# Kernel tuning notes

Measured on AMD Instinct MI355X. Metric: run time of the kernel, lower is better.

The kernel has to match this reference:

```python
import jax, jax.numpy as jnp
import numpy as np

# ---- dims (match init_kwargs) ----
N_E, N_R = 200000, 500
DIM_C, DIM_L, DIM_D = 64, 256, 128
NUM_LAYERS, N_HEADS = 2, 4
FEAT = 2 * DIM_D + DIM_C          # event embedding dim = 320
IN_DIM = FEAT + DIM_D + 1         # attention input: evt + time_emb + ones = 449
DH = FEAT // N_HEADS              # head dim = 80
B, T = 32, 64
TIME_M, TIME_MAX = 1.0, 2000.0
EPS = 1e-8


def setup_inputs() -> dict:
    key = jax.random.key(0)
    ks = jax.random.split(key, 18)
    s = 0.05
    seq_subject = jax.random.randint(ks[0], (B, T), 0, N_E)
    seq_object = jax.random.randint(ks[1], (B, T), 0, N_E)
    seq_relation = jax.random.randint(ks[2], (B, T), 0, N_R)
    # chronological event times
    seq_time = jnp.cumsum(jax.random.uniform(ks[3], (B, T)) * 2.0, axis=1)
    # persistent entity memory buffers
    mem = jax.random.normal(ks[4], (N_E, DIM_D)) * 0.1
    latest_time = jnp.zeros((N_E,), jnp.float32)
    # relation embedding table with padding row (idx N_R) zeroed
    relation_emb = (jax.random.normal(ks[5], (N_R + 1, DIM_C)) * 0.1).at[N_R].set(0.0)
    # RNN entity update params (torch Linear, bias=False; stored as [in,out])
    W_hidden = jax.random.normal(ks[6], (2 * DIM_D + DIM_C, DIM_L)) * s
    W_hh = jax.random.normal(ks[7], (DIM_L, DIM_D)) * s
    W_st = jax.random.normal(ks[8], (DIM_D,)) * s
    W_ot = jax.random.normal(ks[9], (DIM_D,)) * s
    # stacked ANHP multi-head attention params per layer
    att_Wq = jax.random.normal(ks[10], (NUM_LAYERS, IN_DIM, N_HEADS * DH)) * s
    att_Wk = jax.random.normal(ks[11], (NUM_LAYERS, IN_DIM, N_HEADS * DH)) * s
    att_Wv = jax.random.normal(ks[12], (NUM_LAYERS, IN_DIM, N_HEADS * DH)) * s
    att_Wo = jax.random.normal(ks[13], (NUM_LAYERS, N_HEADS * DH, FEAT)) * s
    # score MLP: Linear(FEAT, DIM_D) -> ReLU -> Linear(DIM_D, 1)
    score_W1 = jax.random.normal(ks[14], (FEAT, DIM_D)) * s
    score_b1 = jnp.zeros((DIM_D,), jnp.float32)
    score_W2 = jax.random.normal(ks[15], (DIM_D, 1)) * s
    score_b2 = jnp.zeros((1,), jnp.float32)
    return dict(seq_subject=seq_subject, seq_object=seq_object,
                seq_relation=seq_relation, seq_time=seq_time,
                mem=mem, latest_time=latest_time, relation_emb=relation_emb,
                W_hidden=W_hidden, W_hh=W_hh, W_st=W_st, W_ot=W_ot,
                att_Wq=att_Wq, att_Wk=att_Wk, att_Wv=att_Wv, att_Wo=att_Wo,
                score_W1=score_W1, score_b1=score_b1,
                score_W2=score_W2, score_b2=score_b2)


def _forward(seq_subject, seq_object, seq_relation, seq_time,
             mem, latest_time, relation_emb,
             W_hidden, W_hh, W_st, W_ot,
             att_Wq, att_Wk, att_Wv, att_Wo,
             score_W1, score_b1, score_W2, score_b2):
    # ---- phase 1: sequential gather -> RNN update -> scatter over entity memory ----
    def step(carry, x):
        m, lt = carry
        s, o, r, t = x                      # each [B]
        s_emb = m[s]                        # gather [B, DIM_D]
        o_emb = m[o]
        r_emb = relation_emb[r]             # [B, DIM_C]
        inp = jnp.concatenate([s_emb, o_emb, r_emb], -1)   # [B, 2d+c]
        h = jax.nn.sigmoid(inp @ W_hidden)                  # [B, DIM_L]
        dt_s = t - lt[s]
        dt_o = t - lt[o]
        hh = h @ W_hh                                       # [B, DIM_D]
        new_s = jax.nn.sigmoid(dt_s[:, None] * W_st[None, :] + hh)
        new_o = jax.nn.sigmoid(dt_o[:, None] * W_ot[None, :] + hh)
        m = m.at[s].set(new_s).at[o].set(new_o)             # scatter back
        lt = lt.at[s].set(t).at[o].set(t)
        evt = jnp.concatenate([new_s, new_o, r_emb], -1)    # [B, FEAT]
        return (m, lt), evt

    xs = (seq_subject.T, seq_object.T, seq_relation.T, seq_time.T)  # [T, B]
    (mem, latest_time), evt_seq = jax.lax.scan(step, (mem, latest_time), xs)
    evt = jnp.transpose(evt_seq, (1, 0, 2))                 # [B, T, FEAT]

    # ---- phase 2: temporal attention scoring (causal: event i attends to j < i) ----
    norm = 1.0 / (TIME_M * (5.0 * TIME_MAX / TIME_M) ** jnp.arange(DIM_D, dtype=jnp.float32))
    time_emb = jnp.sin(seq_time[..., None] * norm)          # [B, T, DIM_D]
    ones = jnp.ones(evt.shape[:-1] + (1,), evt.dtype)
    causal = jnp.tril(jnp.ones((T, T), bool), -1)           # strict past mask
    scale = 1.0 / np.sqrt(DH)

    x = evt
    for l in range(NUM_LAYERS):
        e = jnp.concatenate([x, time_emb, ones], -1)        # [B, T, IN_DIM]
        q = (e @ att_Wq[l]).reshape(B, T, N_HEADS, DH)
        k = (e @ att_Wk[l]).reshape(B, T, N_HEADS, DH)
        v = (e @ att_Wv[l]).reshape(B, T, N_HEADS, DH)
        scores = jnp.einsum('bqhd,bkhd->bhqk', q, k) * scale
        scores = jnp.where(causal, scores, -1e9)
        attn = jax.nn.softmax(scores, axis=-1) * causal     # row 0 (no past) -> zero update
        out = jnp.einsum('bhqk,bkhd->bqhd', attn, v).reshape(B, T, N_HEADS * DH)
        x = x + jnp.tanh(out @ att_Wo[l])

    score = (jax.nn.relu(x @ score_W1 + score_b1) @ score_W2 + score_b2)[..., 0]  # [B, T]
    lam = jax.nn.softplus(score)                             # event intensities
    loss = -jnp.log(lam + EPS)
    total_loss = jnp.mean(loss)                              # mean over batch, averaged /T per step
    return total_loss, lam, mem, latest_time


def reference(seq_subject, seq_object, seq_relation, seq_time,
              mem, latest_time, relation_emb,
              W_hidden, W_hh, W_st, W_ot,
              att_Wq, att_Wk, att_Wv, att_Wo,
              score_W1, score_b1, score_W2, score_b2):
    return _forward(seq_subject, seq_object, seq_relation, seq_time,
                    mem, latest_time, relation_emb,
                    W_hidden, W_hh, W_st, W_ot,
                    att_Wq, att_Wk, att_Wv, att_Wo,
                    score_W1, score_b1, score_W2, score_b2)
```

## Files before the change

### kernel.cpp

```cpp
#include <hip/hip_runtime.h>

#define NE   200000
#define DC   64
#define DL   256
#define DD   128
#define FEAT 320
#define IND  449
#define INDP 512
#define DH   80
#define BB   32
#define TT   64
#define NEV  2048
#define NSLOT 4096

typedef __attribute__((ext_vector_type(4))) float  floatx4;
typedef __attribute__((ext_vector_type(4), aligned(4))) float floatx4u;

__device__ __forceinline__ float sigmoidf_(float x) { return 1.0f / (1.0f + __expf(-x)); }

__global__ __launch_bounds__(256)
void copy_init(const float* __restrict__ mem0, const float* __restrict__ lt0,
               float* __restrict__ out_mem, float* __restrict__ out_lt) {
    const size_t NM = (size_t)NE * DD;
    const size_t NL = (size_t)NE;
    size_t gid = (size_t)blockIdx.x * 256 + threadIdx.x;
    size_t stride = (size_t)gridDim.x * 256;
    if (gid == 0) {
        out_mem[0] = mem0[0]; out_mem[1] = mem0[1]; out_mem[2] = mem0[2];
        out_mem[NM - 1] = mem0[NM - 1];
        out_lt[0] = lt0[0]; out_lt[1] = lt0[1]; out_lt[2] = lt0[2];
        out_lt[NL - 1] = lt0[NL - 1];
    }
    const size_t nm4 = (NM - 4) / 4;
    float* __restrict__ dm = out_mem + 3;
    size_t i = gid;
    for (; i + 3 * stride < nm4; i += 4 * stride) {
        size_t i0 = i, i1 = i + stride, i2 = i + 2 * stride, i3 = i + 3 * stride;
        floatx4 lo0 = __builtin_nontemporal_load((const floatx4*)&mem0[i0 * 4]);
        floatx4 hi0 = __builtin_nontemporal_load((const floatx4*)&mem0[i0 * 4 + 4]);
        floatx4 lo1 = __builtin_nontemporal_load((const floatx4*)&mem0[i1 * 4]);
        floatx4 hi1 = __builtin_nontemporal_load((const floatx4*)&mem0[i1 * 4 + 4]);
        floatx4 lo2 = __builtin_nontemporal_load((const floatx4*)&mem0[i2 * 4]);
        floatx4 hi2 = __builtin_nontemporal_load((const floatx4*)&mem0[i2 * 4 + 4]);
        floatx4 lo3 = __builtin_nontemporal_load((const floatx4*)&mem0[i3 * 4]);
        floatx4 hi3 = __builtin_nontemporal_load((const floatx4*)&mem0[i3 * 4 + 4]);
        floatx4 o0 = {lo0[3], hi0[0], hi0[1], hi0[2]};
        floatx4 o1 = {lo1[3], hi1[0], hi1[1], hi1[2]};
        floatx4 o2 = {lo2[3], hi2[0], hi2[1], hi2[2]};
        floatx4 o3 = {lo3[3], hi3[0], hi3[1], hi3[2]};
        __builtin_nontemporal_store(o0, (floatx4*)&dm[i0 * 4]);
        __builtin_nontemporal_store(o1, (floatx4*)&dm[i1 * 4]);
        __builtin_nontemporal_store(o2, (floatx4*)&dm[i2 * 4]);
        __builtin_nontemporal_store(o3, (floatx4*)&dm[i3 * 4]);
    }
    for (; i < nm4; i += stride) {
        floatx4 lo = __builtin_nontemporal_load((const floatx4*)&mem0[i * 4]);
        floatx4 hi = __builtin_nontemporal_load((const floatx4*)&mem0[i * 4 + 4]);
        floatx4 o = {lo[3], hi[0], hi[1], hi[2]};
        __builtin_nontemporal_store(o, (floatx4*)&dm[i * 4]);
    }
    const size_t nl4 = (NL - 4) / 4;
    float* __restrict__ dl = out_lt + 3;
    for (size_t j = gid; j < nl4; j += stride) {
        floatx4 lo = __builtin_nontemporal_load((const floatx4*)&lt0[j * 4]);
        floatx4 hi = __builtin_nontemporal_load((const floatx4*)&lt0[j * 4 + 4]);
        floatx4 o = {lo[3], hi[0], hi[1], hi[2]};
        __builtin_nontemporal_store(o, (floatx4*)&dl[j * 4]);
    }
}

__global__ __launch_bounds__(256)
void slot_analyze(const int* __restrict__ seq_s, const int* __restrict__ seq_o,
                  const float* __restrict__ seq_time, const float* __restrict__ lt0,
                  float* __restrict__ slotDt, int* __restrict__ slotPrev,
                  int* __restrict__ slotWin) {
    __shared__ int entL[NSLOT];
    int tid = threadIdx.x;
    for (int j = tid; j < NSLOT; j += 256) {
        int b = j & 31, side = (j >> 5) & 1, t = j >> 6;
        entL[j] = (side ? seq_o : seq_s)[b * TT + t];
    }
    __syncthreads();
    int wave = tid >> 6, lane = tid & 63;
    int slot = blockIdx.x * 4 + wave;
    int t = slot >> 6;
    int myent = entL[slot];
    int win = 1, best = -1;
#pragma unroll 8
    for (int jj = 0; jj < NSLOT / 64; ++jj) {
        int j = jj * 64 + lane;
        if (entL[j] == myent) {
            if (j > slot) win = 0;
            else if ((j >> 6) < t && j > best) best = j;
        }
    }
#pragma unroll
    for (int off = 32; off; off >>= 1) {
        int ob = __shfl_xor(best, off, 64);
        best = best > ob ? best : ob;
    }
    win = __all(win);
    if (lane == 0) {
        int b = slot & 31;
        float tv = seq_time[b * TT + t];
        float pt = (best >= 0) ? seq_time[(best & 31) * TT + (best >> 6)] : lt0[myent];
        slotDt[slot]   = tv - pt;
        slotPrev[slot] = best;
        slotWin[slot]  = win;
    }
}

__global__ __launch_bounds__(256)
void fixlist_build(const int* __restrict__ slotPrev, int* __restrict__ fixList,
                   int* __restrict__ fixState, int* __restrict__ evFixIdx,
                   int* __restrict__ fixCnt) {
    int e = blockIdx.x * 256 + threadIdx.x;
    int b = e >> 6, t = e & 63;
    int c = (slotPrev[t * 64 + b] >= 0) | (slotPrev[t * 64 + 32 + b] >= 0);
    int idx = -1;
    if (c) { idx = atomicAdd(fixCnt, 1); fixList[idx] = e; fixState[idx] = -1; }
    evFixIdx[e] = idx;
}

__global__ __launch_bounds__(256)
void event_compute(const int* __restrict__ seq_s, const int* __restrict__ seq_o,
                   const int* __restrict__ seq_r, const float* __restrict__ seq_time,
                   const float* __restrict__ mem0, const float* __restrict__ rel,
                   const float* __restrict__ W_hidden, const float* __restrict__ W_hh,
                   const float* __restrict__ W_st, const float* __restrict__ W_ot,
                   const float* __restrict__ slotDt,
                   float* __restrict__ evt, float* __restrict__ ebuf) {
    __shared__ float xc[8][FEAT];
    __shared__ float hs[8][DL];
    __shared__ int   sSi[8], sOi[8], sRi[8];
    __shared__ float sDs[8], sDo[8], sTv[8];
    int tid = threadIdx.x;
    int e0 = blockIdx.x * 8;
    if (tid < 8) {
        int e = e0 + tid;
        sSi[tid] = seq_s[e]; sOi[tid] = seq_o[e]; sRi[tid] = seq_r[e];
        int b = e >> 6, t = e & 63;
        sDs[tid] = slotDt[t * 64 + b];
        sDo[tid] = slotDt[t * 64 + 32 + b];
        sTv[tid] = seq_time[e];
    }
    __syncthreads();
    for (int i = tid; i < 8 * FEAT; i += 256) {
        int r = i / FEAT, k = i - r * FEAT;
        float v;
        if (k < DD)            v = mem0[(size_t)sSi[r] * DD + k];
        else if (k < 2 * DD)   v = mem0[(size_t)sOi[r] * DD + (k - DD)];
        else                   v = rel[(size_t)sRi[r] * DC + (k - 2 * DD)];
        xc[r][k] = v;
    }
    __syncthreads();
    {
        int j = tid;
        float acc[8] = {0.f,0.f,0.f,0.f,0.f,0.f,0.f,0.f};
        for (int k = 0; k < FEAT; ++k) {
            float w = W_hidden[(size_t)k * DL + j];
#pragma unroll
            for (int r = 0; r < 8; ++r) acc[r] += xc[r][k] * w;
        }
#pragma unroll
        for (int r = 0; r < 8; ++r) hs[r][j] = sigmoidf_(acc[r]);
    }
    __syncthreads();
    {
        int d = tid & 127, grp = tid >> 7;
        float acc[4] = {0.f,0.f,0.f,0.f};
        for (int l = 0; l < DL; ++l) {
            float w = W_hh[(size_t)l * DD + d];
#pragma unroll
            for (int rr = 0; rr < 4; ++rr) acc[rr] += hs[grp * 4 + rr][l] * w;
        }
        float wst = W_st[d], wot = W_ot[d];
#pragma unroll
        for (int rr = 0; rr < 4; ++rr) {
            int r = grp * 4 + rr;
            int e = e0 + r;
            float ns  = sigmoidf_(sDs[r] * wst + acc[rr]);
            float no_ = sigmoidf_(sDo[r] * wot + acc[rr]);
            evt[(size_t)e * FEAT + d]      = ns;
            evt[(size_t)e * FEAT + DD + d] = no_;
            ebuf[(size_t)e * INDP + d]      = ns;
            ebuf[(size_t)e * INDP + DD + d] = no_;
        }
    }
    for (int i = tid; i < 8 * DC; i += 256) {
        int r = i >> 6, c = i & 63;
        float v = xc[r][2 * DD + c];
        int e = e0 + r;
        evt[(size_t)e * FEAT + 2 * DD + c] = v;
        ebuf[(size_t)e * INDP + 2 * DD + c] = v;
    }
    for (int i = tid; i < 8 * DD; i += 256) {
        int r = i >> 7, d = i & 127;
        float denom = __powf(1.0e4f, (float)d);
        float v = sinf(sTv[r] * (1.0f / denom));
        int e = e0 + r;
        ebuf[(size_t)e * INDP + FEAT + d] = v;
    }
    if (tid < 8) ebuf[(size_t)(e0 + tid) * INDP + FEAT + DD] = 1.0f;
}

__global__ __launch_bounds__(256)
void fix_round(int round,
               const int* __restrict__ seq_s, const int* __restrict__ seq_o,
               const float* __restrict__ mem0, const float* __restrict__ W_hidden,
               const float* __restrict__ W_hh, const float* __restrict__ W_st,
               const float* __restrict__ W_ot, const float* __restrict__ slotDt,
               const int* __restrict__ slotPrev, const int* __restrict__ fixList,
               int* __restrict__ fixState, const int* __restrict__ evFixIdx,
               const int* __restrict__ fixCnt,
               float* __restrict__ evt, float* __restrict__ ebuf) {
    __shared__ float xc[FEAT];
    __shared__ float hsv[DL];
    __shared__ float hp[2][DD];
    __shared__ int sGo, sPs, sPo, sE;
    int tid = threadIdx.x;
    int n = *fixCnt;
    for (int f = blockIdx.x; f < n; f += gridDim.x) {
        if (tid == 0) {
            int go = 0, ps = 0, po = 0, e = 0;
            if (fixState[f] == -1) {
                e = fixList[f];
                int b = e >> 6, t = e & 63;
                ps = slotPrev[t * 64 + b];
                po = slotPrev[t * 64 + 32 + b];
                go = 1;
                if (ps >= 0) {
                    int pe = (ps & 31) * 64 + (ps >> 6);
                    int fi = evFixIdx[pe];
                    if (fi >= 0) { int st = fixState[fi]; if (st < 0 || st >= round) go = 0; }
                }
                if (po >= 0) {
                    int pe = (po & 31) * 64 + (po >> 6);
                    int fi = evFixIdx[pe];
                    if (fi >= 0) { int st = fixState[fi]; if (st < 0 || st >= round) go = 0; }
                }
            }
            sGo = go; sPs = ps; sPo = po; sE = e;
        }
        __syncthreads();
        int go = sGo, ps = sPs, po = sPo, e = sE;
        __syncthreads();
        if (!go) continue;
        int b = e >> 6, t = e & 63;
        for (int i = tid; i < FEAT; i += 256) {
            float v;
            if (i < DD) {
                v = (ps >= 0) ? evt[(size_t)((ps & 31) * 64 + (ps >> 6)) * FEAT + ((ps >> 5) & 1) * DD + i]
                              : mem0[(size_t)seq_s[e] * DD + i];
            } else if (i < 2 * DD) {
                int k = i - DD;
                v = (po >= 0) ? evt[(size_t)((po & 31) * 64 + (po >> 6)) * FEAT + ((po >> 5) & 1) * DD + k]
                              : mem0[(size_t)seq_o[e] * DD + k];
            } else {
                v = evt[(size_t)e * FEAT + i];
            }
            xc[i] = v;
        }
        __syncthreads();
        {
            float a0 = 0.f, a1 = 0.f, a2 = 0.f, a3 = 0.f;
            for (int k = 0; k < FEAT; k += 4) {
                a0 += xc[k]     * W_hidden[(size_t)k * DL + tid];
                a1 += xc[k + 1] * W_hidden[(size_t)(k + 1) * DL + tid];
                a2 += xc[k + 2] * W_hidden[(size_t)(k + 2) * DL + tid];
                a3 += xc[k + 3] * W_hidden[(size_t)(k + 3) * DL + tid];
            }
            hsv[tid] = sigmoidf_((a0 + a1) + (a2 + a3));
        }
        __syncthreads();
        {
            int d = tid & 127, g = tid >> 7;
            float a0 = 0.f, a1 = 0.f;
            int l0 = g * 128;
            for (int l = 0; l < 128; l += 2) {
                a0 += hsv[l0 + l]     * W_hh[(size_t)(l0 + l) * DD + d];
                a1 += hsv[l0 + l + 1] * W_hh[(size_t)(l0 + l + 1) * DD + d];
            }
            hp[g][d] = a0 + a1;
        }
        __syncthreads();
        if (tid < DD) {
            float hh = hp[0][tid] + hp[1][tid];
            float ns  = sigmoidf_(slotDt[t * 64 + b]      * W_st[tid] + hh);
            float no_ = sigmoidf_(slotDt[t * 64 + 32 + b] * W_ot[tid] + hh);
            evt[(size_t)e * FEAT + tid]      = ns;
            evt[(size_t)e * FEAT + DD + tid] = no_;
            ebuf[(size_t)e * INDP + tid]      = ns;
            ebuf[(size_t)e * INDP + DD + tid] = no_;
        }
        __syncthreads();
        __threadfence();
        if (tid == 0) fixState[f] = round;
        __syncthreads();
    }
}

__global__ __launch_bounds__(256)
void scatter_win(const int* __restrict__ seq_s, const int* __restrict__ seq_o,
                 const float* __restrict__ seq_time, const int* __restrict__ slotWin,
                 const float* __restrict__ evt, float* __restrict__ out_mem,
                 float* __restrict__ out_lt) {
    int gid = blockIdx.x * 256 + threadIdx.x;
    int slot = gid >> 5, c = gid & 31;
    if (!slotWin[slot]) return;
    int b = slot & 31, side = (slot >> 5) & 1, t = slot >> 6;
    int e = b * TT + t;
    int ent = (side ? seq_o : seq_s)[e];
    floatx4 v = *(const floatx4*)&evt[(size_t)e * FEAT + side * DD + c * 4];
    *(floatx4u*)&out_mem[(size_t)ent * DD + c * 4] = v;
    if (c == 0) out_lt[ent] = seq_time[e];
}

__global__ __launch_bounds__(128)
void proj(const float* __restrict__ ebuf, const float* __restrict__ Wq,
          const float* __restrict__ Wk, const float* __restrict__ Wv,
          float* __restrict__ q, float* __restrict__ k, float* __restrict__ v) {
    __shared__ float AsT[2][32][33];
    __shared__ float Bs[2][32][36];
    __shared__ float comb[32][36];
    const float* W = (blockIdx.z == 0) ? Wq : (blockIdx.z == 1) ? Wk : Wv;
    float* out = (blockIdx.z == 0) ? q : (blockIdx.z == 1) ? k : v;
    int tid = threadIdx.x;
    int w = tid >> 6, lane = tid & 63;
    int row0 = blockIdx.x * 32, col0 = blockIdx.y * 32;
    int tx = lane & 7, ty = lane >> 3;
    const int sr = lane >> 3, sk4 = (lane & 7) * 4;
    const int IT0 = w * 8, IT1 = IT0 + 8;
    floatx4 aR[4], bR[4], acc[4];
#pragma unroll
    for (int i = 0; i < 4; ++i) acc[i] = (floatx4){0.f, 0.f, 0.f, 0.f};
#pragma unroll
    for (int m = 0; m < 4; ++m) {
        int r = m * 8 + sr;
        int kg = IT0 * 32 + r;
        aR[m] = *(const floatx4*)&ebuf[(size_t)(row0 + r) * INDP + IT0 * 32 + sk4];
        bR[m] = (kg < IND) ? *(const floatx4*)&W[(size_t)kg * FEAT + col0 + sk4]
                           : (floatx4){0.f, 0.f, 0.f, 0.f};
    }
    for (int it = IT0; it < IT1; ++it) {
        __syncthreads();
#pragma unroll
        for (int m = 0; m < 4; ++m) {
            int r = m * 8 + sr;
            AsT[w][sk4 + 0][r] = aR[m][0];
            AsT[w][sk4 + 1][r] = aR[m][1];
            AsT[w][sk4 + 2][r] = aR[m][2];
            AsT[w][sk4 + 3][r] = aR[m][3];
            *(floatx4*)&Bs[w][r][sk4] = bR[m];
        }
        __syncthreads();
        if (it + 1 < IT1) {
            int k0n = (it + 1) * 32;
#pragma unroll
            for (int m = 0; m < 4; ++m) {
                int r = m * 8 + sr;
                int kg = k0n + r;
                aR[m] = *(const floatx4*)&ebuf[(size_t)(row0 + r) * INDP + k0n + sk4];
                bR[m] = (kg < IND) ? *(const floatx4*)&W[(size_t)kg * FEAT + col0 + sk4]
                                   : (floatx4){0.f, 0.f, 0.f, 0.f};
            }
        }
#pragma unroll
        for (int kk = 0; kk < 32; ++kk) {
            floatx4 a = *(const floatx4*)&AsT[w][kk][ty * 4];
            floatx4 b = *(const floatx4*)&Bs[w][kk][tx * 4];
#pragma unroll
            for (int i = 0; i < 4; ++i) acc[i] += a[i] * b;
        }
    }
    if (w == 1) {
#pragma unroll
        for (int i = 0; i < 4; ++i)
            *(floatx4*)&comb[ty * 4 + i][tx * 4] = acc[i];
    }
    __syncthreads();
    if (w == 0) {
#pragma unroll
        for (int i = 0; i < 4; ++i) {
            floatx4 p = *(const floatx4*)&comb[ty * 4 + i][tx * 4];
            floatx4 s = acc[i] + p;
            *(floatx4*)&out[(size_t)(row0 + ty * 4 + i) * FEAT + col0 + tx * 4] = s;
        }
    }
}

__global__ __launch_bounds__(128)
void outproj(const float* __restrict__ ain, const float* __restrict__ Wo,
             const float* __restrict__ resid, float* __restrict__ xout,
             float* __restrict__ ebufW, int writeE) {
    __shared__ float AsT[2][32][33];
    __shared__ float Bs[2][32][36];
    __shared__ float comb[32][36];
    int tid = threadIdx.x;
    int w = tid >> 6, lane = tid & 63;
    int row0 = blockIdx.x * 32, col0 = blockIdx.y * 32;
    int tx = lane & 7, ty = lane >> 3;
    const int sr = lane >> 3, sk4 = (lane & 7) * 4;
    const int IT0 = w * 5, IT1 = IT0 + 5;
    floatx4 aR[4], bR[4], acc[4];
#pragma unroll
    for (int i = 0; i < 4; ++i) acc[i] = (floatx4){0.f, 0.f, 0.f, 0.f};
#pragma unroll
    for (int m = 0; m < 4; ++m) {
        int r = m * 8 + sr;
        aR[m] = *(const floatx4*)&ain[(size_t)(row0 + r) * FEAT + IT0 * 32 + sk4];
        bR[m] = *(const floatx4*)&Wo[(size_t)(IT0 * 32 + r) * FEAT + col0 + sk4];
    }
    for (int it = IT0; it < IT1; ++it) {
        __syncthreads();
#pragma unroll
        for (int m = 0; m < 4; ++m) {
            int r = m * 8 + sr;
            AsT[w][sk4 + 0][r] = aR[m][0];
            AsT[w][sk4 + 1][r] = aR[m][1];
            AsT[w][sk4 + 2][r] = aR[m][2];
            AsT[w][sk4 + 3][r] = aR[m][3];
            *(floatx4*)&Bs[w][r][sk4] = bR[m];
        }
        __syncthreads();
        if (it + 1 < IT1) {
            int k0n = (it + 1) * 32;
#pragma unroll
            for (int m = 0; m < 4; ++m) {
                int r = m * 8 + sr;
                aR[m] = *(const floatx4*)&ain[(size_t)(row0 + r) * FEAT + k0n + sk4];
                bR[m] = *(const floatx4*)&Wo[(size_t)(k0n + r) * FEAT + col0 + sk4];
            }
        }
#pragma unroll
        for (int kk = 0; kk < 32; ++kk) {
            floatx4 a = *(const floatx4*)&AsT[w][kk][ty * 4];
            floatx4 b = *(const floatx4*)&Bs[w][kk][tx * 4];
#pragma unroll
            for (int i = 0; i < 4; ++i) acc[i] += a[i] * b;
        }
    }
    if (w == 1) {
#pragma unroll
        for (int i = 0; i < 4; ++i)
            *(floatx4*)&comb[ty * 4 + i][tx * 4] = acc[i];
    }
    __syncthreads();
    if (w == 0) {
#pragma unroll
        for (int i = 0; i < 4; ++i) {
            int row = row0 + ty * 4 + i;
            int c0 = col0 + tx * 4;
            floatx4 p = *(const floatx4*)&comb[ty * 4 + i][tx * 4];
            floatx4 a = acc[i] + p;
            floatx4 res = *(const floatx4*)&resid[(size_t)row * FEAT + c0];
            floatx4 o;
#pragma unroll
            for (int j = 0; j < 4; ++j) o[j] = res[j] + tanhf(a[j]);
            *(floatx4*)&xout[(size_t)row * FEAT + c0] = o;
            if (writeE) *(floatx4*)&ebufW[(size_t)row * INDP + c0] = o;
        }
    }
}

__global__ __launch_bounds__(256)
void attn(const float* __restrict__ q, const float* __restrict__ k,
          const float* __restrict__ v, float* __restrict__ ao) {
    __shared__ float qs[TT][DH], ks[TT][DH], vs[TT][DH];
    __shared__ float sc[TT][TT + 1];
    int bh = blockIdx.x;
    int b = bh >> 2, h = bh & 3;
    int tid = threadIdx.x;
    for (int i = tid; i < TT * DH; i += 256) {
        int r = i / DH, d = i - r * DH;
        size_t base = (size_t)(b * TT + r) * FEAT + h * DH + d;
        qs[r][d] = q[base]; ks[r][d] = k[base]; vs[r][d] = v[base];
    }
    __syncthreads();
    const float scale = 0.11180339887498949f;
    for (int idx = tid; idx < TT * TT; idx += 256) {
        int i = idx >> 6, j = idx & 63;
        float s = 0.f;
        for (int d = 0; d < DH; ++d) s += qs[i][d] * ks[j][d];
        sc[i][j] = s * scale;
    }
    __syncthreads();
    if (tid < TT) {
        int i = tid;
        if (i == 0) {
            for (int j = 0; j < TT; ++j) sc[0][j] = 0.0f;
        } else {
            float m = -1e30f;
            for (int j = 0; j < i; ++j) m = fmaxf(m, sc[i][j]);
            float sum = 0.f;
            for (int j = 0; j < i; ++j) { float p = __expf(sc[i][j] - m); sc[i][j] = p; sum += p; }
            float inv = 1.0f / sum;
            for (int j = 0; j < i; ++j) sc[i][j] *= inv;
            for (int j = i; j < TT; ++j) sc[i][j] = 0.0f;
        }
    }
    __syncthreads();
    for (int idx = tid; idx < TT * DH; idx += 256) {
        int i = idx / DH, d = idx - i * DH;
        float s = 0.f;
        for (int j = 0; j < TT; ++j) s += sc[i][j] * vs[j][d];
        ao[(size_t)(b * TT + i) * FEAT + h * DH + d] = s;
    }
}

__global__ __launch_bounds__(128)
void score_k(const float* __restrict__ x, const float* __restrict__ W1,
             const float* __restrict__ b1, const float* __restrict__ W2,
             const float* __restrict__ b2, float* __restrict__ lam_out,
             float* __restrict__ loss_out) {
    __shared__ float xr[FEAT];
    __shared__ float red[2];
    int e = blockIdx.x;
    int tid = threadIdx.x;
    for (int f = tid; f < FEAT; f += 128) xr[f] = x[(size_t)e * FEAT + f];
    __syncthreads();
    int d = tid;
    float acc = b1[d];
    for (int kk = 0; kk < FEAT; ++kk) acc += xr[kk] * W1[kk * DD + d];
    acc = fmaxf(acc, 0.0f) * W2[d];
    for (int off = 32; off; off >>= 1) acc += __shfl_down(acc, off, 64);
    if ((tid & 63) == 0) red[tid >> 6] = acc;
    __syncthreads();
    if (tid == 0) {
        float s = red[0] + red[1] + b2[0];
        float lam = fmaxf(s, 0.0f) + log1pf(expf(-fabsf(s)));
        lam_out[e] = lam;
        atomicAdd(loss_out, -logf(lam + 1e-8f) * (1.0f / 2048.0f));
    }
}

extern "C" void kernel_launch(void* const* d_in, const int* in_sizes, int n_in,
                              void* d_out, int out_size, void* d_ws, size_t ws_size,
                              hipStream_t stream) {
    const int*   seq_s = (const int*)d_in[0];
    const int*   seq_o = (const int*)d_in[1];
    const int*   seq_r = (const int*)d_in[2];
    const float* seq_t = (const float*)d_in[3];
    const float* mem0  = (const float*)d_in[4];
    const float* lt0   = (const float*)d_in[5];
    const float* rel   = (const float*)d_in[6];
    const float* W_hidden = (const float*)d_in[7];
    const float* W_hh  = (const float*)d_in[8];
    const float* W_st  = (const float*)d_in[9];
    const float* W_ot  = (const float*)d_in[10];
    const float* Wq    = (const float*)d_in[11];
    const float* Wk    = (const float*)d_in[12];
    const float* Wv    = (const float*)d_in[13];
    const float* Wo    = (const float*)d_in[14];
    const float* sW1   = (const float*)d_in[15];
    const float* sb1   = (const float*)d_in[16];
    const float* sW2   = (const float*)d_in[17];
    const float* sb2   = (const float*)d_in[18];

    float* out      = (float*)d_out;
    float* out_lam  = out + 1;
    float* out_mem  = out + 2049;
    float* out_lt   = out + 2049 + (size_t)NE * DD;

    float* ws = (float*)d_ws;
    float* evt   = ws;
    float* xbuf  = ws + 655360;
    float* ebuf  = ws + 1310720;
    float* qbuf  = ws + 2359296;
    float* kbuf  = ws + 3014656;
    float* vbuf  = ws + 3670016;
    float* aobuf = ws + 4325376;
    float* slotDt   = ws + 4980736;
    int*   slotPrev = (int*)(ws + 4984832);
    int*   slotWin  = (int*)(ws + 4988928);
    int*   fixList  = (int*)(ws + 4993024);
    int*   fixState = (int*)(ws + 4995072);
    int*   evFixIdx = (int*)(ws + 4997120);
    int*   fixCnt   = (int*)(ws + 4999168);

    hipMemsetAsync(fixCnt, 0, sizeof(int), stream);
    hipMemsetAsync(out, 0, sizeof(float), stream);
    hipMemsetAsync(ebuf, 0, (size_t)NEV * INDP * sizeof(float), stream);

    copy_init<<<2048, 256, 0, stream>>>(mem0, lt0, out_mem, out_lt);

    slot_analyze<<<NSLOT / 4, 256, 0, stream>>>(seq_s, seq_o, seq_t, lt0,
                                                slotDt, slotPrev, slotWin);
    fixlist_build<<<NEV / 256, 256, 0, stream>>>(slotPrev, fixList, fixState,
                                                 evFixIdx, fixCnt);
    event_compute<<<NEV / 8, 256, 0, stream>>>(seq_s, seq_o, seq_r, seq_t, mem0, rel,
                                               W_hidden, W_hh, W_st, W_ot, slotDt,
                                               evt, ebuf);
    for (int r = 0; r < 4; ++r)
        fix_round<<<64, 256, 0, stream>>>(r, seq_s, seq_o, mem0, W_hidden, W_hh,
                                          W_st, W_ot, slotDt, slotPrev,
                                          fixList, fixState, evFixIdx, fixCnt, evt, ebuf);
    scatter_win<<<512, 256, 0, stream>>>(seq_s, seq_o, seq_t, slotWin, evt, out_mem, out_lt);

    for (int l = 0; l < 2; ++l) {
        const float* src = l ? xbuf : evt;
        proj<<<dim3(64, 10, 3), 128, 0, stream>>>(ebuf,
                                                  Wq + (size_t)l * IND * FEAT,
                                                  Wk + (size_t)l * IND * FEAT,
                                                  Wv + (size_t)l * IND * FEAT,
                                                  qbuf, kbuf, vbuf);
        attn<<<128, 256, 0, stream>>>(qbuf, kbuf, vbuf, aobuf);
        outproj<<<dim3(64, 10), 128, 0, stream>>>(aobuf, Wo + (size_t)l * FEAT * FEAT,
                                                  src, xbuf, ebuf, (l == 0) ? 1 : 0);
    }
    score_k<<<NEV, 128, 0, stream>>>(xbuf, sW1, sb1, sW2, sb2, out_lam, out);
}
```

Before: 561.4 us.

## Split attention into query tiles, parallelize softmax with shuffles, pad shared arrays

```diff
diff --git a/kernel.cpp b/kernel.cpp
--- a/kernel.cpp
+++ b/kernel.cpp
@@ -466,45 +466,65 @@
 __global__ __launch_bounds__(256)
 void attn(const float* __restrict__ q, const float* __restrict__ k,
           const float* __restrict__ v, float* __restrict__ ao) {
-    __shared__ float qs[TT][DH], ks[TT][DH], vs[TT][DH];
-    __shared__ float sc[TT][TT + 1];
+    __shared__ float qs[16][80];
+    __shared__ float ks[TT][81];
+    __shared__ float vs[TT][81];
+    __shared__ float sc[16][65];
     int bh = blockIdx.x;
-    int b = bh >> 2, h = bh & 3;
+    int b = bh >> 4, h = (bh >> 2) & 3, qt = bh & 3;
     int tid = threadIdx.x;
     for (int i = tid; i < TT * DH; i += 256) {
         int r = i / DH, d = i - r * DH;
         size_t base = (size_t)(b * TT + r) * FEAT + h * DH + d;
-        qs[r][d] = q[base]; ks[r][d] = k[base]; vs[r][d] = v[base];
+        ks[r][d] = k[base];
+        vs[r][d] = v[base];
+    }
+    for (int i = tid; i < 16 * DH; i += 256) {
+        int r = i / DH, d = i - r * DH;
+        qs[r][d] = q[(size_t)(b * TT + qt * 16 + r) * FEAT + h * DH + d];
     }
     __syncthreads();
     const float scale = 0.11180339887498949f;
-    for (int idx = tid; idx < TT * TT; idx += 256) {
+    for (int idx = tid; idx < 16 * 64; idx += 256) {
         int i = idx >> 6, j = idx & 63;
         float s = 0.f;
+#pragma unroll 8
         for (int d = 0; d < DH; ++d) s += qs[i][d] * ks[j][d];
         sc[i][j] = s * scale;
     }
     __syncthreads();
-    if (tid < TT) {
-        int i = tid;
-        if (i == 0) {
-            for (int j = 0; j < TT; ++j) sc[0][j] = 0.0f;
-        } else {
-            float m = -1e30f;
-            for (int j = 0; j < i; ++j) m = fmaxf(m, sc[i][j]);
-            float sum = 0.f;
-            for (int j = 0; j < i; ++j) { float p = __expf(sc[i][j] - m); sc[i][j] = p; sum += p; }
-            float inv = 1.0f / sum;
-            for (int j = 0; j < i; ++j) sc[i][j] *= inv;
-            for (int j = i; j < TT; ++j) sc[i][j] = 0.0f;
-        }
-    }
-    __syncthreads();
-    for (int idx = tid; idx < TT * DH; idx += 256) {
+    {
+        int r = tid >> 4, l = tid & 15;
+        int qi = qt * 16 + r;
+        float p0, p1, p2, p3;
+        int j0 = l, j1 = l + 16, j2 = l + 32, j3 = l + 48;
+        p0 = (j0 < qi) ? sc[r][j0] : -1e30f;
+        p1 = (j1 < qi) ? sc[r][j1] : -1e30f;
+        p2 = (j2 < qi) ? sc[r][j2] : -1e30f;
+        p3 = (j3 < qi) ? sc[r][j3] : -1e30f;
+        float m = fmaxf(fmaxf(p0, p1), fmaxf(p2, p3));
+#pragma unroll
+        for (int off = 8; off; off >>= 1) m = fmaxf(m, __shfl_xor(m, off, 64));
+        p0 = (j0 < qi) ? __expf(p0 - m) : 0.f;
+        p1 = (j1 < qi) ? __expf(p1 - m) : 0.f;
+        p2 = (j2 < qi) ? __expf(p2 - m) : 0.f;
+        p3 = (j3 < qi) ? __expf(p3 - m) : 0.f;
+        float sum = (p0 + p1) + (p2 + p3);
+#pragma unroll
+        for (int off = 8; off; off >>= 1) sum += __shfl_xor(sum, off, 64);
+        float inv = (qi > 0) ? 1.0f / sum : 0.f;
+        sc[r][j0] = p0 * inv;
+        sc[r][j1] = p1 * inv;
+        sc[r][j2] = p2 * inv;
+        sc[r][j3] = p3 * inv;
+    }
+    __syncthreads();
+    for (int idx = tid; idx < 16 * DH; idx += 256) {
         int i = idx / DH, d = idx - i * DH;
         float s = 0.f;
+#pragma unroll 8
         for (int j = 0; j < TT; ++j) s += sc[i][j] * vs[j][d];
-        ao[(size_t)(b * TT + i) * FEAT + h * DH + d] = s;
+        ao[(size_t)(b * TT + qt * 16 + i) * FEAT + h * DH + d] = s;
     }
 }
 
@@ -604,7 +624,7 @@
                                                   Wk + (size_t)l * IND * FEAT,
                                                   Wv + (size_t)l * IND * FEAT,
                                                   qbuf, kbuf, vbuf);
-        attn<<<128, 256, 0, stream>>>(qbuf, kbuf, vbuf, aobuf);
+        attn<<<512, 256, 0, stream>>>(qbuf, kbuf, vbuf, aobuf);
         outproj<<<dim3(64, 10), 128, 0, stream>>>(aobuf, Wo + (size_t)l * FEAT * FEAT,
                                                   src, xbuf, ebuf, (l == 0) ? 1 : 0);
     }
```

Result: faster. 505.6 us (-9.9%).
